# Kernel optimization log

Measured on AMD Instinct MI355X. Metric: run time of the kernel, lower is better.

The kernel has to match this reference:

```python
import jax, jax.numpy as jnp
import numpy as np

USER_NUM = 100000
ITEM_NUM = 100000  # padding index; table has ITEM_NUM+1 rows
D = 64
B = 4096
L = 200
NEG_WEIGHT = 0.1


def setup_inputs() -> dict:
    key = jax.random.key(0)
    k1, k2, k3, k4, k5 = jax.random.split(key, 5)
    uids = jax.random.randint(k1, (B,), 0, USER_NUM, dtype=jnp.int64 if jax.config.jax_enable_x64 else jnp.int32)
    pos_iids = jax.random.randint(k2, (B, L), 0, ITEM_NUM + 1, dtype=jnp.int64 if jax.config.jax_enable_x64 else jnp.int32)
    user_W = jax.random.normal(k3, (USER_NUM, D), dtype=jnp.float32) * 0.1
    item_W = jax.random.normal(k4, (ITEM_NUM + 1, D), dtype=jnp.float32) * 0.1
    h = jnp.full((D, 1), 0.01, dtype=jnp.float32)  # reset_para: constant 0.01
    return {"uids": uids, "pos_iids": pos_iids, "user_W": user_W, "item_W": item_W, "h": h}


def reference(uids, pos_iids, user_W, item_W, h):
    u_emb = user_W[uids]                      # [B, D] (dropout p=0 -> identity)
    pos_embs = item_W[pos_iids]               # [B, L, D]
    mask = (pos_iids != ITEM_NUM).astype(u_emb.dtype)  # padding id masked out
    pos_embs = pos_embs * mask[:, :, None]
    # hpq[b,l] = sum_d u[b,d] * pos[b,l,d] * h[d]
    hpq = jnp.einsum('bd,bld,d->bl', u_emb, pos_embs, h[:, 0])
    pos_data_loss = jnp.sum((1.0 - NEG_WEIGHT) * jnp.square(hpq) - 2.0 * hpq)
    # part_1/part_2 in torch are sums of per-row outer products == Gram matrices
    part_1 = item_W.T @ item_W                # [D, D]
    part_2 = u_emb.T @ u_emb                  # [D, D]
    part_3 = h @ h.T                          # [D, D]
    all_data_loss = jnp.sum(part_1 * part_2 * part_3)
    return NEG_WEIGHT * all_data_loss + pos_data_loss
```

## Files before the change

### kernel.cpp

```cpp
#include <hip/hip_runtime.h>

#define D 64
#define ITEM_PAD 100000
#define NROW_I (ITEM_PAD + 1)
#define LSEQ 200
#define BATCH 4096
#define NEG_W 0.1f
#define CH 128
#define NBI 256
#define NBU 32
#define GSZ (D * D)
#define LDS_P 66

#define BFT_FLOATS 3200032
#define PITEM_OFF  ((size_t)BFT_FLOATS)
#define PUSER_OFF  (PITEM_OFF + (size_t)NBI * GSZ)
#define POS_OFF    (PUSER_OFF + (size_t)NBU * GSZ)
#define GDOT_OFF   (POS_OFF + BATCH)

typedef short  bf16x8 __attribute__((ext_vector_type(8)));
typedef float  f32x4  __attribute__((ext_vector_type(4)));

__device__ __forceinline__ unsigned short f2bf_rne(float x) {
    unsigned u = __builtin_bit_cast(unsigned, x);
    return (unsigned short)((u + 0x7fffu + ((u >> 16) & 1u)) >> 16);
}
__device__ __forceinline__ float bf_lo(unsigned u) {
    return __builtin_bit_cast(float, u << 16);
}
__device__ __forceinline__ float bf_hi(unsigned u) {
    return __builtin_bit_cast(float, u & 0xffff0000u);
}

__global__ void __launch_bounds__(256)
gram_convert(const int* __restrict__ uids,
             const float* __restrict__ user_W,
             const float* __restrict__ item_W,
             float* __restrict__ ws) {
    __shared__ __align__(16) unsigned char smraw[CH * LDS_P * 2];
    ushort* sm16 = (ushort*)smraw;
    float*  smF  = (float*)smraw;

    const int bid  = blockIdx.x;
    const int t    = threadIdx.x;
    const bool item = (bid < NBI);
    const int b0   = item ? bid : bid - NBI;
    const float* __restrict__ W = item ? item_W : user_W;
    const int nrows  = item ? NROW_I : BATCH;
    const int stride = item ? NBI : NBU;
    const int nch    = (nrows + CH - 1) / CH;
    ushort* __restrict__ bft = (ushort*)ws;
    float*  __restrict__ out = ws + (item ? PITEM_OFF + (size_t)b0 * GSZ
                                          : PUSER_OFF + (size_t)b0 * GSZ);

    const int lane = t & 63;
    const int wv   = t >> 6;
    const int rl   = t >> 4;
    const int c4   = t & 15;

    f32x4 acc[4][4];
    #pragma unroll
    for (int a = 0; a < 4; ++a)
        #pragma unroll
        for (int b = 0; b < 4; ++b)
            #pragma unroll
            for (int r = 0; r < 4; ++r)
                acc[a][b][r] = 0.f;

    float4 v[8];
    int c = b0;
    if (c < nch) {
        #pragma unroll
        for (int i = 0; i < 8; ++i) {
            const int r = c * CH + rl + 16 * i;
            v[i] = make_float4(0.f, 0.f, 0.f, 0.f);
            if (r < nrows) {
                const int src = item ? r : uids[r];
                v[i] = *(const float4*)(W + (size_t)src * D + c4 * 4);
            }
        }
    }

    while (c < nch) {
        __syncthreads();
        #pragma unroll
        for (int i = 0; i < 8; ++i) {
            const int rloc = rl + 16 * i;
            ushort2 lo = { f2bf_rne(v[i].x), f2bf_rne(v[i].y) };
            ushort2 hi = { f2bf_rne(v[i].z), f2bf_rne(v[i].w) };
            *(ushort2*)(sm16 + rloc * LDS_P + c4 * 4)     = lo;
            *(ushort2*)(sm16 + rloc * LDS_P + c4 * 4 + 2) = hi;
            if (item) {
                const int r = c * CH + rloc;
                if (r < nrows) {
                    ushort4 s4 = { lo.x, lo.y, hi.x, hi.y };
                    *(ushort4*)(bft + (size_t)r * D + c4 * 4) = s4;
                }
            }
        }
        __syncthreads();

        const int cn = c + stride;
        #pragma unroll
        for (int i = 0; i < 8; ++i) {
            const int r = cn * CH + rl + 16 * i;
            float4 nv = make_float4(0.f, 0.f, 0.f, 0.f);
            if (cn < nch && r < nrows) {
                const int src = item ? r : uids[r];
                nv = *(const float4*)(W + (size_t)src * D + c4 * 4);
            }
            v[i] = nv;
        }

        const int rbase = wv * 32 + (lane >> 4) * 8;
        const int cl    = lane & 15;
        bf16x8 fr[4];
        #pragma unroll
        for (int a = 0; a < 4; ++a)
            #pragma unroll
            for (int e = 0; e < 8; ++e)
                fr[a][e] = (short)sm16[(rbase + e) * LDS_P + a * 16 + cl];

        #pragma unroll
        for (int a = 0; a < 4; ++a)
            #pragma unroll
            for (int b = 0; b < 4; ++b)
                acc[a][b] = __builtin_amdgcn_mfma_f32_16x16x32_bf16(
                                fr[a], fr[b], acc[a][b], 0, 0, 0);
        c = cn;
    }

    __syncthreads();
#define ACC_WRITE()  { _Pragma("unroll") for (int a = 0; a < 4; ++a) \
                       _Pragma("unroll") for (int b = 0; b < 4; ++b) \
                       _Pragma("unroll") for (int r = 0; r < 4; ++r) \
                         smF[(((a*4+b)*4)+r)*64 + lane] = acc[a][b][r]; }
#define ACC_ADD()    { _Pragma("unroll") for (int a = 0; a < 4; ++a) \
                       _Pragma("unroll") for (int b = 0; b < 4; ++b) \
                       _Pragma("unroll") for (int r = 0; r < 4; ++r) \
                         acc[a][b][r] += smF[(((a*4+b)*4)+r)*64 + lane]; }
    if (wv == 1) ACC_WRITE();
    __syncthreads();
    if (wv == 0) ACC_ADD();
    __syncthreads();
    if (wv == 2) ACC_WRITE();
    __syncthreads();
    if (wv == 0) ACC_ADD();
    __syncthreads();
    if (wv == 3) ACC_WRITE();
    __syncthreads();
    if (wv == 0) { ACC_ADD(); ACC_WRITE(); }
    __syncthreads();
#undef ACC_WRITE
#undef ACC_ADD
    #pragma unroll
    for (int k = 0; k < 4; ++k)
        *(float4*)(out + (t + k * 256) * 4) = *(const float4*)(smF + (t + k * 256) * 4);
}

__global__ void pos_and_reduce(const int* __restrict__ uids,
                               const int* __restrict__ pos_iids,
                               const float* __restrict__ user_W,
                               const float* __restrict__ h,
                               float* __restrict__ ws) {
    const int bid = blockIdx.x;
    const int t   = threadIdx.x;
    const int lane = t & 63;
    const int wave = t >> 6;

    if (bid < BATCH) {
        __shared__ float uh[D];
        __shared__ int   sidx[LSEQ];
        __shared__ float red[4];
        const int b = bid;
        const unsigned short* __restrict__ bft = (const unsigned short*)ws;

        if (t < LSEQ) sidx[t] = pos_iids[(size_t)b * LSEQ + t];
        if (t >= 192) {
            const int j = t - 192;
            uh[j] = user_W[(size_t)uids[b] * D + j] * h[j];
        }
        __syncthreads();

        const int p    = lane >> 3;
        const int q    = lane & 7;
        const int base = wave * 8 + p;

        float u8[8];
        *(float4*)(u8 + 0) = *(const float4*)(uh + q * 8);
        *(float4*)(u8 + 4) = *(const float4*)(uh + q * 8 + 4);

        int ids[7];
        #pragma unroll
        for (int k = 0; k < 7; ++k) {
            const int l = base + 32 * k;
            ids[k] = (l < LSEQ) ? sidx[l] : ITEM_PAD;
        }
        uint4 rows[7];
        #pragma unroll
        for (int k = 0; k < 7; ++k) {
            uint4 v = make_uint4(0u, 0u, 0u, 0u);
            if (ids[k] != ITEM_PAD)
                v = *(const uint4*)(bft + (size_t)ids[k] * D + q * 8);
            rows[k] = v;
        }

        float local = 0.f;
        #pragma unroll
        for (int k = 0; k < 7; ++k) {
            const uint4 v = rows[k];
            float s = bf_lo(v.x)*u8[0] + bf_hi(v.x)*u8[1]
                    + bf_lo(v.y)*u8[2] + bf_hi(v.y)*u8[3]
                    + bf_lo(v.z)*u8[4] + bf_hi(v.z)*u8[5]
                    + bf_lo(v.w)*u8[6] + bf_hi(v.w)*u8[7];
            s += __shfl_xor(s, 1);
            s += __shfl_xor(s, 2);
            s += __shfl_xor(s, 4);
            if (q == 0)
                local += (1.0f - NEG_W) * s * s - 2.0f * s;
        }
        local += __shfl_xor(local, 1);
        local += __shfl_xor(local, 2);
        local += __shfl_xor(local, 4);
        local += __shfl_xor(local, 8);
        local += __shfl_xor(local, 16);
        local += __shfl_xor(local, 32);
        if (lane == 0) red[wave] = local;
        __syncthreads();
        if (t == 0)
            ws[POS_OFF + b] = red[0] + red[1] + red[2] + red[3];
    } else {
        __shared__ float rI[4][16];
        __shared__ float rU[4][16];
        const int bb = bid - BATCH;
        const int kk = t & 15;
        const int ps = t >> 4;
        const int k  = bb * 16 + kk;

        float si = 0.f, su = 0.f;
        #pragma unroll 8
        for (int p = ps; p < NBI; p += 16) si += ws[PITEM_OFF + (size_t)p * GSZ + k];
        #pragma unroll
        for (int p = ps; p < NBU; p += 16) su += ws[PUSER_OFF + (size_t)p * GSZ + k];

        si += __shfl_xor(si, 16); si += __shfl_xor(si, 32);
        su += __shfl_xor(su, 16); su += __shfl_xor(su, 32);
        if (lane < 16) { rI[wave][kk] = si; rU[wave][kk] = su; }
        __syncthreads();

        if (wave == 0) {
            float c = 0.f;
            if (t < 16) {
                const float Gi = rI[0][t] + rI[1][t] + rI[2][t] + rI[3][t];
                const float Gu = rU[0][t] + rU[1][t] + rU[2][t] + rU[3][t];
                const int kg = bb * 16 + t;
                const int i = kg >> 6, j = kg & 63;
                c = NEG_W * Gi * Gu * h[i] * h[j];
            }
            c += __shfl_xor(c, 1);
            c += __shfl_xor(c, 2);
            c += __shfl_xor(c, 4);
            c += __shfl_xor(c, 8);
            if (lane == 0) ws[GDOT_OFF + bb] = c;
        }
    }
}

__global__ void final_sum(const float* __restrict__ ws, float* __restrict__ out) {
    __shared__ float red[4];
    const int t = threadIdx.x;
    float s = 0.f;
    #pragma unroll
    for (int k = 0; k < 17; ++k)
        s += ws[POS_OFF + t + k * 256];
    s += __shfl_xor(s, 1);
    s += __shfl_xor(s, 2);
    s += __shfl_xor(s, 4);
    s += __shfl_xor(s, 8);
    s += __shfl_xor(s, 16);
    s += __shfl_xor(s, 32);
    const int lane = t & 63, wave = t >> 6;
    if (lane == 0) red[wave] = s;
    __syncthreads();
    if (t == 0) out[0] = red[0] + red[1] + red[2] + red[3];
}

extern "C" void kernel_launch(void* const* d_in, const int* in_sizes, int n_in,
                              void* d_out, int out_size, void* d_ws, size_t ws_size,
                              hipStream_t stream) {
    const int*   uids     = (const int*)d_in[0];
    const int*   pos_iids = (const int*)d_in[1];
    const float* user_W   = (const float*)d_in[2];
    const float* item_W   = (const float*)d_in[3];
    const float* h        = (const float*)d_in[4];
    float* out = (float*)d_out;
    float* ws  = (float*)d_ws;

    gram_convert<<<NBI + NBU, 256, 0, stream>>>(uids, user_W, item_W, ws);
    pos_and_reduce<<<BATCH + 256, 256, 0, stream>>>(uids, pos_iids, user_W, h, ws);
    final_sum<<<1, 256, 0, stream>>>(ws, out);
}
```

Before: 121.7 us.

## Fuse Gram and positive-score kernels, gather fp32 item rows directly

Drops the bf16 copy of the item table that the Gram kernel wrote for the positive-score pass. The positive-score pass now gathers fp32 rows straight from item_W and runs as extra blocks of the same launch as the Gram blocks. The Gram partial reduction moves into its own small kernel. This removes about 12.8MB of bf16 table writes and lets the two workloads overlap, at the cost of gathering twice as many bytes per positive item (fp32 instead of bf16).

```diff
diff --git a/kernel.cpp b/kernel.cpp
--- a/kernel.cpp
+++ b/kernel.cpp
@@ -9,11 +9,11 @@
 #define CH 128
 #define NBI 256
 #define NBU 32
+#define NGRAM (NBI + NBU)
 #define GSZ (D * D)
 #define LDS_P 66
 
-#define BFT_FLOATS 3200032
-#define PITEM_OFF  ((size_t)BFT_FLOATS)
+#define PITEM_OFF  ((size_t)0)
 #define PUSER_OFF  (PITEM_OFF + (size_t)NBI * GSZ)
 #define POS_OFF    (PUSER_OFF + (size_t)NBU * GSZ)
 #define GDOT_OFF   (POS_OFF + BATCH)
@@ -25,112 +25,100 @@
     unsigned u = __builtin_bit_cast(unsigned, x);
     return (unsigned short)((u + 0x7fffu + ((u >> 16) & 1u)) >> 16);
 }
-__device__ __forceinline__ float bf_lo(unsigned u) {
-    return __builtin_bit_cast(float, u << 16);
-}
-__device__ __forceinline__ float bf_hi(unsigned u) {
-    return __builtin_bit_cast(float, u & 0xffff0000u);
-}
-
-__global__ void __launch_bounds__(256)
-gram_convert(const int* __restrict__ uids,
-             const float* __restrict__ user_W,
-             const float* __restrict__ item_W,
-             float* __restrict__ ws) {
+
+__global__ void gram_and_pos(const int* __restrict__ uids,
+                             const int* __restrict__ pos_iids,
+                             const float* __restrict__ user_W,
+                             const float* __restrict__ item_W,
+                             const float* __restrict__ h,
+                             float* __restrict__ ws) {
     __shared__ __align__(16) unsigned char smraw[CH * LDS_P * 2];
-    ushort* sm16 = (ushort*)smraw;
-    float*  smF  = (float*)smraw;
-
-    const int bid  = blockIdx.x;
-    const int t    = threadIdx.x;
-    const bool item = (bid < NBI);
-    const int b0   = item ? bid : bid - NBI;
-    const float* __restrict__ W = item ? item_W : user_W;
-    const int nrows  = item ? NROW_I : BATCH;
-    const int stride = item ? NBI : NBU;
-    const int nch    = (nrows + CH - 1) / CH;
-    ushort* __restrict__ bft = (ushort*)ws;
-    float*  __restrict__ out = ws + (item ? PITEM_OFF + (size_t)b0 * GSZ
-                                          : PUSER_OFF + (size_t)b0 * GSZ);
-
+    const int bid = blockIdx.x;
+    const int t   = threadIdx.x;
     const int lane = t & 63;
     const int wv   = t >> 6;
-    const int rl   = t >> 4;
-    const int c4   = t & 15;
-
-    f32x4 acc[4][4];
-    #pragma unroll
-    for (int a = 0; a < 4; ++a)
-        #pragma unroll
-        for (int b = 0; b < 4; ++b)
-            #pragma unroll
-            for (int r = 0; r < 4; ++r)
-                acc[a][b][r] = 0.f;
-
-    float4 v[8];
-    int c = b0;
-    if (c < nch) {
-        #pragma unroll
-        for (int i = 0; i < 8; ++i) {
-            const int r = c * CH + rl + 16 * i;
-            v[i] = make_float4(0.f, 0.f, 0.f, 0.f);
-            if (r < nrows) {
-                const int src = item ? r : uids[r];
-                v[i] = *(const float4*)(W + (size_t)src * D + c4 * 4);
-            }
-        }
-    }
-
-    while (c < nch) {
-        __syncthreads();
-        #pragma unroll
-        for (int i = 0; i < 8; ++i) {
-            const int rloc = rl + 16 * i;
-            ushort2 lo = { f2bf_rne(v[i].x), f2bf_rne(v[i].y) };
-            ushort2 hi = { f2bf_rne(v[i].z), f2bf_rne(v[i].w) };
-            *(ushort2*)(sm16 + rloc * LDS_P + c4 * 4)     = lo;
-            *(ushort2*)(sm16 + rloc * LDS_P + c4 * 4 + 2) = hi;
-            if (item) {
-                const int r = c * CH + rloc;
+
+    if (bid < NGRAM) {
+        ushort* sm16 = (ushort*)smraw;
+        float*  smF  = (float*)smraw;
+
+        const bool item = (bid < NBI);
+        const int b0   = item ? bid : bid - NBI;
+        const float* __restrict__ W = item ? item_W : user_W;
+        const int nrows  = item ? NROW_I : BATCH;
+        const int stride = item ? NBI : NBU;
+        const int nch    = (nrows + CH - 1) / CH;
+        float* __restrict__ out = ws + (item ? PITEM_OFF + (size_t)b0 * GSZ
+                                             : PUSER_OFF + (size_t)b0 * GSZ);
+        const int rl = t >> 4;
+        const int c4 = t & 15;
+
+        f32x4 acc[4][4];
+        #pragma unroll
+        for (int a = 0; a < 4; ++a)
+            #pragma unroll
+            for (int b = 0; b < 4; ++b)
+                #pragma unroll
+                for (int r = 0; r < 4; ++r)
+                    acc[a][b][r] = 0.f;
+
+        float4 v[8];
+        int c = b0;
+        if (c < nch) {
+            #pragma unroll
+            for (int i = 0; i < 8; ++i) {
+                const int r = c * CH + rl + 16 * i;
+                v[i] = make_float4(0.f, 0.f, 0.f, 0.f);
                 if (r < nrows) {
-                    ushort4 s4 = { lo.x, lo.y, hi.x, hi.y };
-                    *(ushort4*)(bft + (size_t)r * D + c4 * 4) = s4;
+                    const int src = item ? r : uids[r];
+                    v[i] = *(const float4*)(W + (size_t)src * D + c4 * 4);
                 }
             }
         }
-        __syncthreads();
-
-        const int cn = c + stride;
-        #pragma unroll
-        for (int i = 0; i < 8; ++i) {
-            const int r = cn * CH + rl + 16 * i;
-            float4 nv = make_float4(0.f, 0.f, 0.f, 0.f);
-            if (cn < nch && r < nrows) {
-                const int src = item ? r : uids[r];
-                nv = *(const float4*)(W + (size_t)src * D + c4 * 4);
-            }
-            v[i] = nv;
-        }
-
-        const int rbase = wv * 32 + (lane >> 4) * 8;
-        const int cl    = lane & 15;
-        bf16x8 fr[4];
-        #pragma unroll
-        for (int a = 0; a < 4; ++a)
-            #pragma unroll
-            for (int e = 0; e < 8; ++e)
-                fr[a][e] = (short)sm16[(rbase + e) * LDS_P + a * 16 + cl];
-
-        #pragma unroll
-        for (int a = 0; a < 4; ++a)
-            #pragma unroll
-            for (int b = 0; b < 4; ++b)
-                acc[a][b] = __builtin_amdgcn_mfma_f32_16x16x32_bf16(
-                                fr[a], fr[b], acc[a][b], 0, 0, 0);
-        c = cn;
-    }
-
-    __syncthreads();
+
+        while (c < nch) {
+            __syncthreads();
+            #pragma unroll
+            for (int i = 0; i < 8; ++i) {
+                const int rloc = rl + 16 * i;
+                ushort2 lo = { f2bf_rne(v[i].x), f2bf_rne(v[i].y) };
+                ushort2 hi = { f2bf_rne(v[i].z), f2bf_rne(v[i].w) };
+                *(ushort2*)(sm16 + rloc * LDS_P + c4 * 4)     = lo;
+                *(ushort2*)(sm16 + rloc * LDS_P + c4 * 4 + 2) = hi;
+            }
+            __syncthreads();
+
+            const int cn = c + stride;
+            #pragma unroll
+            for (int i = 0; i < 8; ++i) {
+                const int r = cn * CH + rl + 16 * i;
+                float4 nv = make_float4(0.f, 0.f, 0.f, 0.f);
+                if (cn < nch && r < nrows) {
+                    const int src = item ? r : uids[r];
+                    nv = *(const float4*)(W + (size_t)src * D + c4 * 4);
+                }
+                v[i] = nv;
+            }
+
+            const int rbase = wv * 32 + (lane >> 4) * 8;
+            const int cl    = lane & 15;
+            bf16x8 fr[4];
+            #pragma unroll
+            for (int a = 0; a < 4; ++a)
+                #pragma unroll
+                for (int e = 0; e < 8; ++e)
+                    fr[a][e] = (short)sm16[(rbase + e) * LDS_P + a * 16 + cl];
+
+            #pragma unroll
+            for (int a = 0; a < 4; ++a)
+                #pragma unroll
+                for (int b = 0; b < 4; ++b)
+                    acc[a][b] = __builtin_amdgcn_mfma_f32_16x16x32_bf16(
+                                    fr[a], fr[b], acc[a][b], 0, 0, 0);
+            c = cn;
+        }
+
+        __syncthreads();
 #define ACC_WRITE()  { _Pragma("unroll") for (int a = 0; a < 4; ++a) \
                        _Pragma("unroll") for (int b = 0; b < 4; ++b) \
                        _Pragma("unroll") for (int r = 0; r < 4; ++r) \
@@ -139,41 +127,28 @@
                        _Pragma("unroll") for (int b = 0; b < 4; ++b) \
                        _Pragma("unroll") for (int r = 0; r < 4; ++r) \
                          acc[a][b][r] += smF[(((a*4+b)*4)+r)*64 + lane]; }
-    if (wv == 1) ACC_WRITE();
-    __syncthreads();
-    if (wv == 0) ACC_ADD();
-    __syncthreads();
-    if (wv == 2) ACC_WRITE();
-    __syncthreads();
-    if (wv == 0) ACC_ADD();
-    __syncthreads();
-    if (wv == 3) ACC_WRITE();
-    __syncthreads();
-    if (wv == 0) { ACC_ADD(); ACC_WRITE(); }
-    __syncthreads();
+        if (wv == 1) ACC_WRITE();
+        __syncthreads();
+        if (wv == 0) ACC_ADD();
+        __syncthreads();
+        if (wv == 2) ACC_WRITE();
+        __syncthreads();
+        if (wv == 0) ACC_ADD();
+        __syncthreads();
+        if (wv == 3) ACC_WRITE();
+        __syncthreads();
+        if (wv == 0) { ACC_ADD(); ACC_WRITE(); }
+        __syncthreads();
 #undef ACC_WRITE
 #undef ACC_ADD
-    #pragma unroll
-    for (int k = 0; k < 4; ++k)
-        *(float4*)(out + (t + k * 256) * 4) = *(const float4*)(smF + (t + k * 256) * 4);
-}
-
-__global__ void pos_and_reduce(const int* __restrict__ uids,
-                               const int* __restrict__ pos_iids,
-                               const float* __restrict__ user_W,
-                               const float* __restrict__ h,
-                               float* __restrict__ ws) {
-    const int bid = blockIdx.x;
-    const int t   = threadIdx.x;
-    const int lane = t & 63;
-    const int wave = t >> 6;
-
-    if (bid < BATCH) {
-        __shared__ float uh[D];
-        __shared__ int   sidx[LSEQ];
-        __shared__ float red[4];
-        const int b = bid;
-        const unsigned short* __restrict__ bft = (const unsigned short*)ws;
+        #pragma unroll
+        for (int k = 0; k < 4; ++k)
+            *(float4*)(out + (t + k * 256) * 4) = *(const float4*)(smF + (t + k * 256) * 4);
+    } else {
+        float* uh   = (float*)smraw;
+        int*   sidx = (int*)(smraw + 256);
+        float* red  = (float*)(smraw + 256 + 800);
+        const int b = bid - NGRAM;
 
         if (t < LSEQ) sidx[t] = pos_iids[(size_t)b * LSEQ + t];
         if (t >= 192) {
@@ -184,7 +159,7 @@
 
         const int p    = lane >> 3;
         const int q    = lane & 7;
-        const int base = wave * 8 + p;
+        const int base = wv * 8 + p;
 
         float u8[8];
         *(float4*)(u8 + 0) = *(const float4*)(uh + q * 8);
@@ -196,23 +171,25 @@
             const int l = base + 32 * k;
             ids[k] = (l < LSEQ) ? sidx[l] : ITEM_PAD;
         }
-        uint4 rows[7];
+        float4 ra[7], rb[7];
         #pragma unroll
         for (int k = 0; k < 7; ++k) {
-            uint4 v = make_uint4(0u, 0u, 0u, 0u);
-            if (ids[k] != ITEM_PAD)
-                v = *(const uint4*)(bft + (size_t)ids[k] * D + q * 8);
-            rows[k] = v;
+            ra[k] = make_float4(0.f, 0.f, 0.f, 0.f);
+            rb[k] = make_float4(0.f, 0.f, 0.f, 0.f);
+            if (ids[k] != ITEM_PAD) {
+                const float* row = item_W + (size_t)ids[k] * D + q * 8;
+                ra[k] = *(const float4*)(row);
+                rb[k] = *(const float4*)(row + 4);
+            }
         }
 
         float local = 0.f;
         #pragma unroll
         for (int k = 0; k < 7; ++k) {
-            const uint4 v = rows[k];
-            float s = bf_lo(v.x)*u8[0] + bf_hi(v.x)*u8[1]
-                    + bf_lo(v.y)*u8[2] + bf_hi(v.y)*u8[3]
-                    + bf_lo(v.z)*u8[4] + bf_hi(v.z)*u8[5]
-                    + bf_lo(v.w)*u8[6] + bf_hi(v.w)*u8[7];
+            float s = ra[k].x * u8[0] + ra[k].y * u8[1]
+                    + ra[k].z * u8[2] + ra[k].w * u8[3]
+                    + rb[k].x * u8[4] + rb[k].y * u8[5]
+                    + rb[k].z * u8[6] + rb[k].w * u8[7];
             s += __shfl_xor(s, 1);
             s += __shfl_xor(s, 2);
             s += __shfl_xor(s, 4);
@@ -225,44 +202,49 @@
         local += __shfl_xor(local, 8);
         local += __shfl_xor(local, 16);
         local += __shfl_xor(local, 32);
-        if (lane == 0) red[wave] = local;
+        if (lane == 0) red[wv] = local;
         __syncthreads();
         if (t == 0)
             ws[POS_OFF + b] = red[0] + red[1] + red[2] + red[3];
-    } else {
-        __shared__ float rI[4][16];
-        __shared__ float rU[4][16];
-        const int bb = bid - BATCH;
-        const int kk = t & 15;
-        const int ps = t >> 4;
-        const int k  = bb * 16 + kk;
-
-        float si = 0.f, su = 0.f;
-        #pragma unroll 8
-        for (int p = ps; p < NBI; p += 16) si += ws[PITEM_OFF + (size_t)p * GSZ + k];
-        #pragma unroll
-        for (int p = ps; p < NBU; p += 16) su += ws[PUSER_OFF + (size_t)p * GSZ + k];
-
-        si += __shfl_xor(si, 16); si += __shfl_xor(si, 32);
-        su += __shfl_xor(su, 16); su += __shfl_xor(su, 32);
-        if (lane < 16) { rI[wave][kk] = si; rU[wave][kk] = su; }
-        __syncthreads();
-
-        if (wave == 0) {
-            float c = 0.f;
-            if (t < 16) {
-                const float Gi = rI[0][t] + rI[1][t] + rI[2][t] + rI[3][t];
-                const float Gu = rU[0][t] + rU[1][t] + rU[2][t] + rU[3][t];
-                const int kg = bb * 16 + t;
-                const int i = kg >> 6, j = kg & 63;
-                c = NEG_W * Gi * Gu * h[i] * h[j];
-            }
-            c += __shfl_xor(c, 1);
-            c += __shfl_xor(c, 2);
-            c += __shfl_xor(c, 4);
-            c += __shfl_xor(c, 8);
-            if (lane == 0) ws[GDOT_OFF + bb] = c;
-        }
+    }
+}
+
+__global__ void gram_dot(const float* __restrict__ h, float* __restrict__ ws) {
+    __shared__ float rI[4][16];
+    __shared__ float rU[4][16];
+    const int bb = blockIdx.x;
+    const int t  = threadIdx.x;
+    const int lane = t & 63;
+    const int wave = t >> 6;
+    const int kk = t & 15;
+    const int ps = t >> 4;
+    const int k  = bb * 16 + kk;
+
+    float si = 0.f, su = 0.f;
+    #pragma unroll 8
+    for (int p = ps; p < NBI; p += 16) si += ws[PITEM_OFF + (size_t)p * GSZ + k];
+    #pragma unroll
+    for (int p = ps; p < NBU; p += 16) su += ws[PUSER_OFF + (size_t)p * GSZ + k];
+
+    si += __shfl_xor(si, 16); si += __shfl_xor(si, 32);
+    su += __shfl_xor(su, 16); su += __shfl_xor(su, 32);
+    if (lane < 16) { rI[wave][kk] = si; rU[wave][kk] = su; }
+    __syncthreads();
+
+    if (wave == 0) {
+        float c = 0.f;
+        if (t < 16) {
+            const float Gi = rI[0][t] + rI[1][t] + rI[2][t] + rI[3][t];
+            const float Gu = rU[0][t] + rU[1][t] + rU[2][t] + rU[3][t];
+            const int kg = bb * 16 + t;
+            const int i = kg >> 6, j = kg & 63;
+            c = NEG_W * Gi * Gu * h[i] * h[j];
+        }
+        c += __shfl_xor(c, 1);
+        c += __shfl_xor(c, 2);
+        c += __shfl_xor(c, 4);
+        c += __shfl_xor(c, 8);
+        if (lane == 0) ws[GDOT_OFF + bb] = c;
     }
 }
 
@@ -296,7 +278,7 @@
     float* out = (float*)d_out;
     float* ws  = (float*)d_ws;
 
-    gram_convert<<<NBI + NBU, 256, 0, stream>>>(uids, user_W, item_W, ws);
-    pos_and_reduce<<<BATCH + 256, 256, 0, stream>>>(uids, pos_iids, user_W, h, ws);
+    gram_and_pos<<<NGRAM + BATCH, 256, 0, stream>>>(uids, pos_iids, user_W, item_W, h, ws);
+    gram_dot<<<256, 256, 0, stream>>>(h, ws);
     final_sum<<<1, 256, 0, stream>>>(ws, out);
 }
```

New measurement: 123.1 us. About the same (+1.1%).
